# Kernel optimization log

Measured on AMD Instinct MI355X. Metric: run time of the kernel, lower is better.

Reference implementation:

```python
import jax, jax.numpy as jnp
import numpy as np

NEG_SLOPE = 0.2
EPS = 1e-16

N_NODES = 32768
N_EDGES = 160000
DIM = 768
HEADS1 = 4
OUT1 = DIM // HEADS1  # 192 per head, concat -> 768
HEADS2 = 1
OUT2 = DIM
N_REL = 3


def setup_inputs() -> dict:
    key = jax.random.key(0)
    ks = jax.random.split(key, 12)
    s = 0.02
    return {
        "x": jax.random.normal(ks[0], (N_NODES, DIM), dtype=jnp.float32),
        "edge_index": jax.random.randint(ks[1], (2, N_EDGES), 0, N_NODES, dtype=jnp.int64),
        "edge_type": jax.random.randint(ks[2], (N_EDGES,), 0, N_REL, dtype=jnp.int64),
        "W1": jax.random.normal(ks[3], (N_REL, DIM, HEADS1 * OUT1), dtype=jnp.float32) * s,
        "q1": jax.random.normal(ks[4], (HEADS1 * OUT1, HEADS1), dtype=jnp.float32) * s,
        "k1": jax.random.normal(ks[5], (HEADS1 * OUT1, HEADS1), dtype=jnp.float32) * s,
        "b1": jnp.zeros((HEADS1 * OUT1,), dtype=jnp.float32),
        "W2": jax.random.normal(ks[6], (N_REL, DIM, HEADS2 * OUT2), dtype=jnp.float32) * s,
        "q2": jax.random.normal(ks[7], (HEADS2 * OUT2, HEADS2), dtype=jnp.float32) * s,
        "k2": jax.random.normal(ks[8], (HEADS2 * OUT2, HEADS2), dtype=jnp.float32) * s,
        "b2": jnp.zeros((HEADS2 * OUT2,), dtype=jnp.float32),
    }


def rgat_conv(x, W, q, k, b, src, dst, etype, heads, out_ch, n_nodes):
    """PyG RGATConv, additive-self-attention, across-relation, concat=True, eval mode."""
    # per-relation transform of all nodes: [R, N, H*O] (avoids [E, in, H*O] weight gather)
    xr = jnp.einsum('nd,rdf->rnf', x, W)
    oi = xr[etype, dst]                      # [E, H*O] transformed target feats
    oj = xr[etype, src]                      # [E, H*O] transformed source feats
    qi = oi @ q                              # [E, H]
    kj = oj @ k                              # [E, H]
    alpha = jax.nn.leaky_relu(qi + kj, NEG_SLOPE)
    # segment softmax over edges sharing the same target node
    m = jax.ops.segment_max(alpha, dst, num_segments=n_nodes)     # [N, H]
    e = jnp.exp(alpha - m[dst])
    z = jax.ops.segment_sum(e, dst, num_segments=n_nodes)         # [N, H]
    a = e / (z[dst] + EPS)                                        # [E, H]
    msg = (a[:, :, None] * oj.reshape(-1, heads, out_ch)).reshape(-1, heads * out_ch)
    out = jax.ops.segment_sum(msg, dst, num_segments=n_nodes)     # [N, H*O]
    return out + b


def reference(x, edge_index, edge_type, W1, q1, k1, b1, W2, q2, k2, b2):
    src, dst = edge_index[0], edge_index[1]
    n = x.shape[0]
    h = rgat_conv(x, W1, q1, k1, b1, src, dst, edge_type, HEADS1, OUT1, n)
    h = jax.nn.elu(h)
    # dropout is identity in eval mode
    out = rgat_conv(h, W2, q2, k2, b2, src, dst, edge_type, HEADS2, OUT2, n)
    return out
```

## Files before the change

kernel.cpp:

```cpp
#include <hip/hip_runtime.h>


#define DIM   768
#define NREL  3

typedef __bf16 bf16x8 __attribute__((ext_vector_type(8)));
typedef float  f32x4  __attribute__((ext_vector_type(4)));
typedef float  f32x16 __attribute__((ext_vector_type(16)));
typedef unsigned short us4 __attribute__((ext_vector_type(4)));
typedef unsigned short us8 __attribute__((ext_vector_type(8)));

__device__ __forceinline__ float bfs(unsigned short u){
  union { unsigned u; float f; } v; v.u = ((unsigned)u) << 16; return v.f;
}
__device__ __forceinline__ float bfl(unsigned x){
  union { unsigned u; float f; } v; v.u = x << 16; return v.f;
}
__device__ __forceinline__ float bfh(unsigned x){
  union { unsigned u; float f; } v; v.u = x & 0xffff0000u; return v.f;
}
__device__ __forceinline__ unsigned short f2bf(float f){
  union { float f; unsigned u; } v; v.f = f;
  unsigned r = v.u + 0x7fffu + ((v.u >> 16) & 1u);
  return (unsigned short)(r >> 16);
}
__device__ __forceinline__ unsigned pck(float a, float b){
  return (unsigned)f2bf(a) | ((unsigned)f2bf(b) << 16);
}
__device__ __forceinline__ float ldf(const void* p, size_t i, int is32){
  return is32 ? ((const float*)p)[i] : bfs(((const unsigned short*)p)[i]);
}
__device__ __forceinline__ int ldi(const void* p, size_t i, int is64){
  return is64 ? ((const int*)p)[2 * i] : ((const int*)p)[i];
}

typedef __attribute__((address_space(1))) void gvoid_t;
typedef __attribute__((address_space(3))) void lvoid_t;
__device__ __forceinline__ void gload16(const void* g, void* l){
  __builtin_amdgcn_global_load_lds((gvoid_t*)g, (lvoid_t*)l, 16, 0, 0);
}

template<int H>
__device__ __forceinline__ float sel(const float (&a)[H], int h){
  float v = a[0];
#pragma unroll
  for (int i = 1; i < H; ++i) v = (h == i) ? a[i] : v;
  return v;
}

__global__ void detect_kernel(const unsigned short* __restrict__ xu,
                              const unsigned* __restrict__ eiu,
                              const unsigned* __restrict__ etyu,
                              int* __restrict__ flags){
  __shared__ int s_weird, s_ei, s_ety;
  int t = threadIdx.x;
  if (t == 0){ s_weird = 0; s_ei = 0; s_ety = 0; }
  __syncthreads();
  unsigned short u = xu[2 * t];
  int ex = (u >> 7) & 0xff;
  if (ex >= 0xF0 || ex <= 0x40) atomicAdd(&s_weird, 1);
  if (t < 128){
    if (eiu[2 * t + 1]  != 0) atomicAdd(&s_ei, 1);
    if (etyu[2 * t + 1] != 0) atomicAdd(&s_ety, 1);
  }
  __syncthreads();
  if (t == 0){
    flags[0] = (s_weird > 16) ? 1 : 0;
    flags[1] = (s_ei  == 0) ? 1 : 0;
    flags[2] = (s_ety == 0) ? 1 : 0;
  }
}

__global__ void convert_x(const void* __restrict__ xin, unsigned short* __restrict__ xb,
                          const int* __restrict__ flags, int n4){
  int i = blockIdx.x * blockDim.x + threadIdx.x;
  if (i >= n4) return;
  if (flags[0]){
    float4 v = ((const float4*)xin)[i];
    us4 o; o.x = f2bf(v.x); o.y = f2bf(v.y); o.z = f2bf(v.z); o.w = f2bf(v.w);
    ((us4*)xb)[i] = o;
  } else {
    ((us4*)xb)[i] = ((const us4*)xin)[i];
  }
}

__global__ void hist_kernel(const void* __restrict__ ei, int* __restrict__ counts,
                            const int* __restrict__ flags, int E){
  int e = blockIdx.x * blockDim.x + threadIdx.x;
  if (e < E) atomicAdd(&counts[ldi(ei, (size_t)E + e, flags[1])], 1);
}

__global__ void scan_kernel(const int* __restrict__ counts, int* __restrict__ offs,
                            int* __restrict__ cursor, int n){
  __shared__ int s[1024];
  int tid = threadIdx.x;
  int base = tid * 32;
  int loc[32];
  int run = 0;
#pragma unroll
  for (int i = 0; i < 32; ++i){ loc[i] = run; run += counts[base + i]; }
  s[tid] = run;
  __syncthreads();
  for (int off = 1; off < 1024; off <<= 1){
    int add = (tid >= off) ? s[tid - off] : 0;
    __syncthreads();
    s[tid] += add;
    __syncthreads();
  }
  int ex = (tid == 0) ? 0 : s[tid - 1];
#pragma unroll
  for (int i = 0; i < 32; ++i){
    int o = ex + loc[i];
    offs[base + i]   = o;
    cursor[base + i] = o;
  }
  if (tid == 1023) offs[n] = s[1023];
}

__global__ void scatter_kernel(const void* __restrict__ ei, const void* __restrict__ ety,
                               int* __restrict__ cursor, int* __restrict__ payload,
                               const int* __restrict__ flags, int E){
  int e = blockIdx.x * blockDim.x + threadIdx.x;
  if (e < E){
    int dst = ldi(ei, (size_t)E + e, flags[1]);
    int src = ldi(ei, (size_t)e,     flags[1]);
    int et  = ldi(ety, (size_t)e,    flags[2]);
    int pos = atomicAdd(&cursor[dst], 1);
    payload[pos] = (et << 16) | src;
  }
}

__global__ void transpose_w(const void* __restrict__ W, unsigned short* __restrict__ Wt,
                            const int* __restrict__ flags){
  __shared__ unsigned short t[32][33];
  int is32 = flags[0];
  int r = blockIdx.z;
  size_t Wb = (size_t)r * DIM * DIM;
  unsigned short* Wd = Wt + (size_t)r * DIM * DIM;
  int tx = threadIdx.x, ty = threadIdx.y;
  int x  = blockIdx.x * 32 + tx;
  int y0 = blockIdx.y * 32;
#pragma unroll
  for (int i = 0; i < 32; i += 8)
    t[ty + i][tx] = f2bf(ldf(W, Wb + (size_t)(y0 + ty + i) * DIM + x, is32));
  __syncthreads();
  int x2 = blockIdx.y * 32 + tx;
  int y2 = blockIdx.x * 32;
#pragma unroll
  for (int i = 0; i < 32; i += 8) Wd[(size_t)(y2 + ty + i) * DIM + x2] = t[tx][ty + i];
}

template<int H>
__global__ void wqk_kernel(const void* __restrict__ W,
                           const void* __restrict__ q, const void* __restrict__ k,
                           unsigned short* __restrict__ Wqkb,
                           const int* __restrict__ flags){
  int is32 = flags[0];
  int wid  = (blockIdx.x * blockDim.x + threadIdx.x) >> 6;
  int lane = threadIdx.x & 63;
  int r = wid / DIM, d = wid % DIM;
  size_t Wrow = ((size_t)r * DIM + d) * DIM;
  float aq[H], ak[H];
#pragma unroll
  for (int h = 0; h < H; ++h){ aq[h] = 0.f; ak[h] = 0.f; }
#pragma unroll
  for (int j = 0; j < 12; ++j){
    int f = j * 64 + lane;
    float wv = ldf(W, Wrow + f, is32);
#pragma unroll
    for (int h = 0; h < H; ++h){
      aq[h] += wv * ldf(q, (size_t)f * H + h, is32);
      ak[h] += wv * ldf(k, (size_t)f * H + h, is32);
    }
  }
#pragma unroll
  for (int h = 0; h < H; ++h){
    for (int off = 32; off; off >>= 1){
      aq[h] += __shfl_xor(aq[h], off);
      ak[h] += __shfl_xor(ak[h], off);
    }
  }
  if (lane == 0){
#pragma unroll
    for (int h = 0; h < H; ++h){
      Wqkb[(size_t)d * 32 + r * 8 + h]     = f2bf(aq[h]);
      Wqkb[(size_t)d * 32 + r * 8 + 4 + h] = f2bf(ak[h]);
    }
  }
}

__global__ void pack_b(const unsigned short* __restrict__ Wqkb, unsigned short* __restrict__ Bpk){
  int i = blockIdx.x * 256 + threadIdx.x;
  if (i >= 3072) return;
  int lane = i & 63, nt = (i >> 6) & 1, t = i >> 7;
  int kb = t * 32 + (lane >> 4) * 8;
  int col = nt * 16 + (lane & 15);
  us8 v;
#pragma unroll
  for (int j = 0; j < 8; ++j) v[j] = Wqkb[(size_t)(kb + j) * 32 + col];
  ((us8*)Bpk)[i] = v;
}

__global__ void __launch_bounds__(256)
qnkn_mfma(const unsigned short* __restrict__ X, const unsigned short* __restrict__ Bpk,
          float* __restrict__ qn, float* __restrict__ kn, int nN){
  int wv = threadIdx.x >> 6, lane = threadIdx.x & 63;
  int row0 = (blockIdx.x * 4 + wv) * 16;
  int ar = lane & 15, quad = lane >> 4;
  const unsigned short* Arow = X + (size_t)(row0 + ar) * DIM + quad * 8;
  const bf16x8* Bp = (const bf16x8*)Bpk;
  f32x4 acc0 = {0.f,0.f,0.f,0.f}, acc1 = {0.f,0.f,0.f,0.f};
#pragma unroll
  for (int t = 0; t < 24; ++t){
    bf16x8 a  = *(const bf16x8*)(Arow + t * 32);
    bf16x8 b0 = Bp[(t * 2 + 0) * 64 + lane];
    bf16x8 b1 = Bp[(t * 2 + 1) * 64 + lane];
    acc0 = __builtin_amdgcn_mfma_f32_16x16x32_bf16(a, b0, acc0, 0, 0, 0);
    acc1 = __builtin_amdgcn_mfma_f32_16x16x32_bf16(a, b1, acc1, 0, 0, 0);
  }
#pragma unroll
  for (int nt = 0; nt < 2; ++nt){
    int col = nt * 16 + (lane & 15);
    if (col < 24){
      int r = col >> 3, isK = (col >> 2) & 1, h = col & 3;
      float* bp = isK ? kn : qn;
      f32x4 a = nt ? acc1 : acc0;
#pragma unroll
      for (int j = 0; j < 4; ++j){
        int row = row0 + quad * 4 + j;
        bp[((size_t)r * nN + row) * 4 + h] = a[j];
      }
    }
  }
}

#define MF(A_, B_, C_) __builtin_amdgcn_mfma_f32_32x32x16_bf16(A_, B_, C_, 0, 0, 0)

#define STAGE(SW, KW) {                                                       \
  gload16(gAa + (KW),            &lds[(SW)*24576 +         wB]);              \
  gload16(gAa +  64*DIM + (KW),  &lds[(SW)*24576 +  4096 + wB]);              \
  gload16(gAa + 128*DIM + (KW),  &lds[(SW)*24576 +  8192 + wB]);              \
  gload16(gAa + 192*DIM + (KW),  &lds[(SW)*24576 + 12288 + wB]);              \
  gload16(gBb + (KW),            &lds[(SW)*24576 + 16384 + wB]);              \
  gload16(gBb +  64*DIM + (KW),  &lds[(SW)*24576 + 20480 + wB]);              \
}

#define STEP(S, KW, DOST) {                                                   \
  if (DOST) STAGE(((S)+2)%3, KW);                                             \
  bf16x8 b00 = *(const bf16x8*)&lds[(S)*24576 + boff0];                       \
  bf16x8 b01 = *(const bf16x8*)&lds[(S)*24576 + boff1];                       \
  bf16x8 b10 = *(const bf16x8*)&lds[(S)*24576 + boff0 + 2048];                \
  bf16x8 b11 = *(const bf16x8*)&lds[(S)*24576 + boff1 + 2048];                \
  bf16x8 a00 = *(const bf16x8*)&lds[(S)*24576 + aoff0];                       \
  bf16x8 a01 = *(const bf16x8*)&lds[(S)*24576 + aoff1];                       \
  bf16x8 a10 = *(const bf16x8*)&lds[(S)*24576 + aoff0 + 2048];                \
  bf16x8 a11 = *(const bf16x8*)&lds[(S)*24576 + aoff1 + 2048];                \
  bf16x8 a20 = *(const bf16x8*)&lds[(S)*24576 + aoff0 + 4096];                \
  bf16x8 a21 = *(const bf16x8*)&lds[(S)*24576 + aoff1 + 4096];                \
  bf16x8 a30 = *(const bf16x8*)&lds[(S)*24576 + aoff0 + 6144];                \
  bf16x8 a31 = *(const bf16x8*)&lds[(S)*24576 + aoff1 + 6144];                \
  __builtin_amdgcn_s_setprio(1);                                              \
  acc[0][0] = MF(a00, b00, acc[0][0]); acc[0][1] = MF(a00, b10, acc[0][1]);   \
  acc[1][0] = MF(a10, b00, acc[1][0]); acc[1][1] = MF(a10, b10, acc[1][1]);   \
  acc[2][0] = MF(a20, b00, acc[2][0]); acc[2][1] = MF(a20, b10, acc[2][1]);   \
  acc[3][0] = MF(a30, b00, acc[3][0]); acc[3][1] = MF(a30, b10, acc[3][1]);   \
  acc[0][0] = MF(a01, b01, acc[0][0]); acc[0][1] = MF(a01, b11, acc[0][1]);   \
  acc[1][0] = MF(a11, b01, acc[1][0]); acc[1][1] = MF(a11, b11, acc[1][1]);   \
  acc[2][0] = MF(a21, b01, acc[2][0]); acc[2][1] = MF(a21, b11, acc[2][1]);   \
  acc[3][0] = MF(a31, b01, acc[3][0]); acc[3][1] = MF(a31, b11, acc[3][1]);   \
  __builtin_amdgcn_s_setprio(0);                                              \
}
#define W6 { asm volatile("s_waitcnt vmcnt(6)" ::: "memory"); __builtin_amdgcn_s_barrier(); }

__global__ void __launch_bounds__(256, 2)
gemm_bf16(const unsigned short* __restrict__ A,
          const unsigned short* __restrict__ Bt,
          unsigned short* __restrict__ C, int M){
  __shared__ __align__(16) unsigned char lds[73728];
  const int K = DIM;
  int i = blockIdx.x;
  int xcd = i & 7, s = i >> 3;
  int bm  = xcd * 16 + s / 18;
  int bnr = s % 18;
  int rrel = bnr / 6, bn = bnr % 6;
  int tid = threadIdx.x;
  int w = tid >> 6, lane = tid & 63;
  int wr = w >> 1, wc = w & 1;
  int lo = lane & 31, hi = lane >> 5;

  int jl   = lo >> 1, rlow = lo & 1, e7 = jl & 7;
  int p0   = (rlow * 4 + hi)     ^ e7;
  int p1   = (rlow * 4 + 2 + hi) ^ e7;
  int aoff0 = (wr * 64 + jl) * 128 + p0 * 16;
  int aoff1 = (wr * 64 + jl) * 128 + p1 * 16;
  int boff0 = 16384 + (wc * 32 + jl) * 128 + p0 * 16;
  int boff1 = 16384 + (wc * 32 + jl) * 128 + p1 * 16;

  int sq   = (tid & 7) ^ ((tid >> 3) & 7);
  int srow = 2 * (tid >> 3) + (sq >> 2);
  const unsigned short* gAa = A  + ((size_t)bm * 256 + srow) * K + (sq & 3) * 8;
  const unsigned short* gBb = Bt + ((size_t)(rrel * DIM + bn * 128 + srow)) * K + (sq & 3) * 8;
  int wB = w * 1024;

  f32x16 acc[4][2];
  f32x16 zz = {0.f,0.f,0.f,0.f,0.f,0.f,0.f,0.f,0.f,0.f,0.f,0.f,0.f,0.f,0.f,0.f};
#pragma unroll
  for (int a = 0; a < 4; ++a){ acc[a][0] = zz; acc[a][1] = zz; }

  STAGE(0, 0); STAGE(1, 32);
  W6;

#pragma unroll 1
  for (int t7 = 0; t7 < 7; ++t7){
    int kb = t7 * 96;
    STEP(0, kb + 64,  1); W6;
    STEP(1, kb + 96,  1); W6;
    STEP(2, kb + 128, 1); W6;
  }
  STEP(0, 736, 1); W6;
  STEP(1, 0, 0);
  asm volatile("s_waitcnt vmcnt(0)" ::: "memory");
  __builtin_amdgcn_s_barrier();
  STEP(2, 0, 0);

  unsigned short* Cg = C + ((size_t)rrel * M + (size_t)bm * 256) * DIM + bn * 128;
#pragma unroll
  for (int mi = 0; mi < 4; ++mi)
#pragma unroll
    for (int ni = 0; ni < 2; ++ni)
#pragma unroll
      for (int rg = 0; rg < 4; ++rg)
#pragma unroll
        for (int j = 0; j < 4; ++j){
          int row = wr * 128 + mi * 32 + rg * 8 + hi * 4 + j;
          int col = wc * 64 + ni * 32 + lo;
          Cg[(size_t)row * DIM + col] = f2bf(acc[mi][ni][rg * 4 + j]);
        }
}

template<int H, bool ELU, bool OUT32>
__global__ void __launch_bounds__(256)
agg_kernel(const unsigned short* __restrict__ xr,
           const float* __restrict__ qn, const float* __restrict__ kn,
           const int* __restrict__ offs, const int* __restrict__ payload,
           const void* __restrict__ bias,
           void* __restrict__ outp,
           const int* __restrict__ flags, int nN, int E){
  const int WH = (H == 4) ? 4 : 1;
  __shared__ int   pay_s[4][64];
  __shared__ float w_s[4][64 * WH];
  int is32 = flags[0];
  int wv   = threadIdx.x >> 6;
  int lane = threadIdx.x & 63;
  int n = blockIdx.x * 4 + wv;
  int rs = offs[n], re = offs[n + 1];
  rs = max(rs, 0); re = min(re, E);
  const int myh = (H == 1) ? 0 : (lane >> 4);

  float m_run[H], z_run[H], acc[12];
#pragma unroll
  for (int h = 0; h < H; ++h){ m_run[h] = -__builtin_inff(); z_run[h] = 0.f; }
#pragma unroll
  for (int i = 0; i < 12; ++i) acc[i] = 0.f;

  for (int base = rs; base < re; base += 64){
    int dc = min(64, re - base);
    int pay = 0;
    float al[H];
#pragma unroll
    for (int h = 0; h < H; ++h) al[h] = -__builtin_inff();
    if (lane < dc){
      pay = payload[base + lane];
      int et = pay >> 16, src = pay & 0xffff;
      if (H == 4){
        f32x4 qv = *(const f32x4*)(qn + ((size_t)et * nN + n)   * 4);
        f32x4 kv = *(const f32x4*)(kn + ((size_t)et * nN + src) * 4);
#pragma unroll
        for (int h = 0; h < H; ++h){
          float a = qv[h & 3] + kv[h & 3];
          al[h] = (a > 0.f) ? a : 0.2f * a;
        }
      } else {
        float a = qn[((size_t)et * nN + n) * 4] + kn[((size_t)et * nN + src) * 4];
        al[0] = (a > 0.f) ? a : 0.2f * a;
      }
    }
    float scs[H], wgt[H];
#pragma unroll
    for (int h = 0; h < H; ++h){
      float v = al[h];
      for (int off = 32; off; off >>= 1) v = fmaxf(v, __shfl_xor(v, off));
      float nm = fmaxf(m_run[h], v);
      scs[h] = (m_run[h] == -__builtin_inff()) ? 0.f : expf(m_run[h] - nm);
      m_run[h] = nm;
      wgt[h] = (lane < dc) ? expf(al[h] - nm) : 0.f;
      float s = wgt[h];
      for (int off = 32; off; off >>= 1) s += __shfl_xor(s, off);
      z_run[h] = z_run[h] * scs[h] + s;
    }
    float msc = sel<H>(scs, myh);
#pragma unroll
    for (int i = 0; i < 12; ++i) acc[i] *= msc;

    if (lane < dc){
      pay_s[wv][lane] = pay;
#pragma unroll
      for (int h = 0; h < WH; ++h) w_s[wv][lane * WH + h] = wgt[h];
    }

    for (int j0 = 0; j0 < dc; j0 += 4){
      uint2 c[4][3];
      float w4[4];
#pragma unroll
      for (int u = 0; u < 4; ++u){
        int jc = j0 + u;
        int ok = jc < dc;
        int jl2 = ok ? jc : j0;
        int pj = pay_s[wv][jl2];
        float ww = w_s[wv][jl2 * WH + ((H == 1) ? 0 : myh)];
        w4[u] = ok ? ww : 0.f;
        int et = pj >> 16, src = pj & 0xffff;
        const uint2* rp = (const uint2*)(xr + ((size_t)et * nN + src) * DIM + lane * 12);
        c[u][0] = rp[0]; c[u][1] = rp[1]; c[u][2] = rp[2];
      }
#pragma unroll
      for (int u = 0; u < 4; ++u){
        float wj = w4[u];
        acc[0]  += wj * bfl(c[u][0].x); acc[1]  += wj * bfh(c[u][0].x);
        acc[2]  += wj * bfl(c[u][0].y); acc[3]  += wj * bfh(c[u][0].y);
        acc[4]  += wj * bfl(c[u][1].x); acc[5]  += wj * bfh(c[u][1].x);
        acc[6]  += wj * bfl(c[u][1].y); acc[7]  += wj * bfh(c[u][1].y);
        acc[8]  += wj * bfl(c[u][2].x); acc[9]  += wj * bfh(c[u][2].x);
        acc[10] += wj * bfl(c[u][2].y); acc[11] += wj * bfh(c[u][2].y);
      }
    }
  }

  float inv = 1.0f / (sel<H>(z_run, myh) + 1e-16f);
  float o[12];
#pragma unroll
  for (int i = 0; i < 12; ++i){
    float v = acc[i] * inv + ldf(bias, (size_t)lane * 12 + i, is32);
    if (ELU) v = (v > 0.f) ? v : (expf(v) - 1.f);
    o[i] = v;
  }
  if (OUT32 && is32){
    float* op = (float*)outp + (size_t)n * DIM + lane * 12;
    float4 f0 = {o[0], o[1], o[2],  o[3]};
    float4 f1 = {o[4], o[5], o[6],  o[7]};
    float4 f2 = {o[8], o[9], o[10], o[11]};
    ((float4*)op)[0] = f0; ((float4*)op)[1] = f1; ((float4*)op)[2] = f2;
  } else {
    uint2* op = (uint2*)((unsigned short*)outp + (size_t)n * DIM + lane * 12);
    uint2 s0, s1, s2;
    s0.x = pck(o[0], o[1]);  s0.y = pck(o[2], o[3]);
    s1.x = pck(o[4], o[5]);  s1.y = pck(o[6], o[7]);
    s2.x = pck(o[8], o[9]);  s2.y = pck(o[10], o[11]);
    op[0] = s0; op[1] = s1; op[2] = s2;
  }
}

extern "C" void kernel_launch(void* const* d_in, const int* in_sizes, int n_in,
                              void* d_out, int out_size, void* d_ws, size_t ws_size,
                              hipStream_t stream){
  const void* x   = d_in[0];
  const void* ei  = d_in[1];
  const void* ety = d_in[2];
  const void* W1  = d_in[3];
  const void* q1  = d_in[4];
  const void* k1  = d_in[5];
  const void* b1  = d_in[6];
  const void* W2  = d_in[7];
  const void* q2  = d_in[8];
  const void* k2  = d_in[9];
  const void* b2  = d_in[10];

  int nN = in_sizes[0] / DIM;
  int E  = in_sizes[2];

  char* ws = (char*)d_ws;
  size_t off = 0;
  auto alloc = [&](size_t bytes) -> void* {
    void* p = ws + off;
    off += (bytes + 255) & ~(size_t)255;
    return p;
  };
  unsigned short* xr   = (unsigned short*)alloc((size_t)NREL * nN * DIM * 2);
  unsigned short* xb   = (unsigned short*)alloc((size_t)nN * DIM * 2);
  unsigned short* h    = (unsigned short*)alloc((size_t)nN * DIM * 2);
  unsigned short* Wt   = (unsigned short*)alloc((size_t)NREL * DIM * DIM * 2);
  unsigned short* Wqkb = (unsigned short*)alloc((size_t)DIM * 32 * 2);
  unsigned short* Bpk  = (unsigned short*)alloc((size_t)3072 * 16);
  float* qn  = (float*)alloc((size_t)NREL * nN * 4 * 4);
  float* kn  = (float*)alloc((size_t)NREL * nN * 4 * 4);
  int* offs    = (int*)alloc((size_t)(nN + 1) * 4);
  int* cursor  = (int*)alloc((size_t)nN * 4);
  int* counts  = (int*)alloc((size_t)nN * 4);
  int* payload = (int*)alloc((size_t)E * 4);
  int* flags   = (int*)alloc(16);

  detect_kernel<<<1, 256, 0, stream>>>((const unsigned short*)x, (const unsigned*)ei,
                                       (const unsigned*)ety, flags);
  convert_x<<<(nN * DIM / 4 + 255) / 256, 256, 0, stream>>>(x, xb, flags, nN * DIM / 4);

  hipMemsetAsync(counts, 0, (size_t)nN * 4, stream);
  hist_kernel<<<(E + 255) / 256, 256, 0, stream>>>(ei, counts, flags, E);
  scan_kernel<<<1, 1024, 0, stream>>>(counts, offs, cursor, nN);
  scatter_kernel<<<(E + 255) / 256, 256, 0, stream>>>(ei, ety, cursor, payload, flags, E);

  dim3 tg(DIM / 32, DIM / 32, NREL), tb(32, 8);
  int gemm_blocks = 8 * (16 * 18);

  transpose_w<<<tg, tb, 0, stream>>>(W1, Wt, flags);
  hipMemsetAsync(Wqkb, 0, (size_t)DIM * 32 * 2, stream);
  wqk_kernel<4><<<(NREL * DIM) / 4, 256, 0, stream>>>(W1, q1, k1, Wqkb, flags);
  pack_b<<<12, 256, 0, stream>>>(Wqkb, Bpk);
  qnkn_mfma<<<nN / 64, 256, 0, stream>>>(xb, Bpk, qn, kn, nN);
  gemm_bf16<<<gemm_blocks, 256, 0, stream>>>(xb, Wt, xr, nN);
  agg_kernel<4, true, false><<<nN / 4, 256, 0, stream>>>(xr, qn, kn, offs, payload, b1, h,
                                                         flags, nN, E);

  transpose_w<<<tg, tb, 0, stream>>>(W2, Wt, flags);
  hipMemsetAsync(Wqkb, 0, (size_t)DIM * 32 * 2, stream);
  wqk_kernel<1><<<(NREL * DIM) / 4, 256, 0, stream>>>(W2, q2, k2, Wqkb, flags);
  pack_b<<<12, 256, 0, stream>>>(Wqkb, Bpk);
  qnkn_mfma<<<nN / 64, 256, 0, stream>>>(h, Bpk, qn, kn, nN);
  gemm_bf16<<<gemm_blocks, 256, 0, stream>>>(h, Wt, xr, nN);
  agg_kernel<1, false, true><<<nN / 4, 256, 0, stream>>>(xr, qn, kn, offs, payload, b2,
                                                         d_out, flags, nN, E);
}
```

Measured before the change: 661.3 us.

## Enlarge GEMM block tile to 256x256 with 4x4 MFMA accumulators per wave

```diff
diff --git a/kernel.cpp b/kernel.cpp
--- a/kernel.cpp
+++ b/kernel.cpp
@@ -236,104 +236,117 @@
 
 #define MF(A_, B_, C_) __builtin_amdgcn_mfma_f32_32x32x16_bf16(A_, B_, C_, 0, 0, 0)
 
-#define STAGE(SW, KW) {                                                       \
-  gload16(gAa + (KW),            &lds[(SW)*24576 +         wB]);              \
-  gload16(gAa +  64*DIM + (KW),  &lds[(SW)*24576 +  4096 + wB]);              \
-  gload16(gAa + 128*DIM + (KW),  &lds[(SW)*24576 +  8192 + wB]);              \
-  gload16(gAa + 192*DIM + (KW),  &lds[(SW)*24576 + 12288 + wB]);              \
-  gload16(gBb + (KW),            &lds[(SW)*24576 + 16384 + wB]);              \
-  gload16(gBb +  64*DIM + (KW),  &lds[(SW)*24576 + 20480 + wB]);              \
-}
-
-#define STEP(S, KW, DOST) {                                                   \
-  if (DOST) STAGE(((S)+2)%3, KW);                                             \
-  bf16x8 b00 = *(const bf16x8*)&lds[(S)*24576 + boff0];                       \
-  bf16x8 b01 = *(const bf16x8*)&lds[(S)*24576 + boff1];                       \
-  bf16x8 b10 = *(const bf16x8*)&lds[(S)*24576 + boff0 + 2048];                \
-  bf16x8 b11 = *(const bf16x8*)&lds[(S)*24576 + boff1 + 2048];                \
-  bf16x8 a00 = *(const bf16x8*)&lds[(S)*24576 + aoff0];                       \
-  bf16x8 a01 = *(const bf16x8*)&lds[(S)*24576 + aoff1];                       \
-  bf16x8 a10 = *(const bf16x8*)&lds[(S)*24576 + aoff0 + 2048];                \
-  bf16x8 a11 = *(const bf16x8*)&lds[(S)*24576 + aoff1 + 2048];                \
-  bf16x8 a20 = *(const bf16x8*)&lds[(S)*24576 + aoff0 + 4096];                \
-  bf16x8 a21 = *(const bf16x8*)&lds[(S)*24576 + aoff1 + 4096];                \
-  bf16x8 a30 = *(const bf16x8*)&lds[(S)*24576 + aoff0 + 6144];                \
-  bf16x8 a31 = *(const bf16x8*)&lds[(S)*24576 + aoff1 + 6144];                \
-  __builtin_amdgcn_s_setprio(1);                                              \
-  acc[0][0] = MF(a00, b00, acc[0][0]); acc[0][1] = MF(a00, b10, acc[0][1]);   \
-  acc[1][0] = MF(a10, b00, acc[1][0]); acc[1][1] = MF(a10, b10, acc[1][1]);   \
-  acc[2][0] = MF(a20, b00, acc[2][0]); acc[2][1] = MF(a20, b10, acc[2][1]);   \
-  acc[3][0] = MF(a30, b00, acc[3][0]); acc[3][1] = MF(a30, b10, acc[3][1]);   \
-  acc[0][0] = MF(a01, b01, acc[0][0]); acc[0][1] = MF(a01, b11, acc[0][1]);   \
-  acc[1][0] = MF(a11, b01, acc[1][0]); acc[1][1] = MF(a11, b11, acc[1][1]);   \
-  acc[2][0] = MF(a21, b01, acc[2][0]); acc[2][1] = MF(a21, b11, acc[2][1]);   \
-  acc[3][0] = MF(a31, b01, acc[3][0]); acc[3][1] = MF(a31, b11, acc[3][1]);   \
-  __builtin_amdgcn_s_setprio(0);                                              \
-}
-#define W6 { asm volatile("s_waitcnt vmcnt(6)" ::: "memory"); __builtin_amdgcn_s_barrier(); }
-
-__global__ void __launch_bounds__(256, 2)
+#define STAGE(SW, KW) {                                                        \
+  gload16(gAa + (KW),                 &lds[(SW)*32768 +         wB]);          \
+  gload16(gAa + (KW) + 16,            &lds[(SW)*32768 +  8192 + wB]);          \
+  gload16(gAa + 128*DIM + (KW),       &lds[(SW)*32768 +  4096 + wB]);          \
+  gload16(gAa + 128*DIM + (KW) + 16,  &lds[(SW)*32768 + 12288 + wB]);          \
+  gload16(gBb + (KW),                 &lds[(SW)*32768 + 16384 + wB]);          \
+  gload16(gBb + (KW) + 16,            &lds[(SW)*32768 + 24576 + wB]);          \
+  gload16(gBb + 128*DIM + (KW),       &lds[(SW)*32768 + 20480 + wB]);          \
+  gload16(gBb + 128*DIM + (KW) + 16,  &lds[(SW)*32768 + 28672 + wB]);          \
+}
+
+#define STEP(S, KW, DOST) {                                                    \
+  if (DOST) STAGE(((S)+2)%3, KW);                                              \
+  bf16x8 a00 = *(const bf16x8*)&lds[(S)*32768 + aoff];                         \
+  bf16x8 a01 = *(const bf16x8*)&lds[(S)*32768 + aoff + 1024];                  \
+  bf16x8 a02 = *(const bf16x8*)&lds[(S)*32768 + aoff + 2048];                  \
+  bf16x8 a03 = *(const bf16x8*)&lds[(S)*32768 + aoff + 3072];                  \
+  bf16x8 b00 = *(const bf16x8*)&lds[(S)*32768 + boff];                         \
+  bf16x8 b01 = *(const bf16x8*)&lds[(S)*32768 + boff + 1024];                  \
+  bf16x8 b02 = *(const bf16x8*)&lds[(S)*32768 + boff + 2048];                  \
+  bf16x8 b03 = *(const bf16x8*)&lds[(S)*32768 + boff + 3072];                  \
+  bf16x8 a10 = *(const bf16x8*)&lds[(S)*32768 + 8192 + aoff];                  \
+  bf16x8 a11 = *(const bf16x8*)&lds[(S)*32768 + 8192 + aoff + 1024];           \
+  bf16x8 a12 = *(const bf16x8*)&lds[(S)*32768 + 8192 + aoff + 2048];           \
+  bf16x8 a13 = *(const bf16x8*)&lds[(S)*32768 + 8192 + aoff + 3072];           \
+  bf16x8 b10 = *(const bf16x8*)&lds[(S)*32768 + 8192 + boff];                  \
+  bf16x8 b11 = *(const bf16x8*)&lds[(S)*32768 + 8192 + boff + 1024];           \
+  bf16x8 b12 = *(const bf16x8*)&lds[(S)*32768 + 8192 + boff + 2048];           \
+  bf16x8 b13 = *(const bf16x8*)&lds[(S)*32768 + 8192 + boff + 3072];           \
+  __builtin_amdgcn_s_setprio(1);                                               \
+  acc[0][0] = MF(a00, b00, acc[0][0]); acc[0][1] = MF(a00, b01, acc[0][1]);    \
+  acc[0][2] = MF(a00, b02, acc[0][2]); acc[0][3] = MF(a00, b03, acc[0][3]);    \
+  acc[1][0] = MF(a01, b00, acc[1][0]); acc[1][1] = MF(a01, b01, acc[1][1]);    \
+  acc[1][2] = MF(a01, b02, acc[1][2]); acc[1][3] = MF(a01, b03, acc[1][3]);    \
+  acc[2][0] = MF(a02, b00, acc[2][0]); acc[2][1] = MF(a02, b01, acc[2][1]);    \
+  acc[2][2] = MF(a02, b02, acc[2][2]); acc[2][3] = MF(a02, b03, acc[2][3]);    \
+  acc[3][0] = MF(a03, b00, acc[3][0]); acc[3][1] = MF(a03, b01, acc[3][1]);    \
+  acc[3][2] = MF(a03, b02, acc[3][2]); acc[3][3] = MF(a03, b03, acc[3][3]);    \
+  acc[0][0] = MF(a10, b10, acc[0][0]); acc[0][1] = MF(a10, b11, acc[0][1]);    \
+  acc[0][2] = MF(a10, b12, acc[0][2]); acc[0][3] = MF(a10, b13, acc[0][3]);    \
+  acc[1][0] = MF(a11, b10, acc[1][0]); acc[1][1] = MF(a11, b11, acc[1][1]);    \
+  acc[1][2] = MF(a11, b12, acc[1][2]); acc[1][3] = MF(a11, b13, acc[1][3]);    \
+  acc[2][0] = MF(a12, b10, acc[2][0]); acc[2][1] = MF(a12, b11, acc[2][1]);    \
+  acc[2][2] = MF(a12, b12, acc[2][2]); acc[2][3] = MF(a12, b13, acc[2][3]);    \
+  acc[3][0] = MF(a13, b10, acc[3][0]); acc[3][1] = MF(a13, b11, acc[3][1]);    \
+  acc[3][2] = MF(a13, b12, acc[3][2]); acc[3][3] = MF(a13, b13, acc[3][3]);    \
+  __builtin_amdgcn_s_setprio(0);                                               \
+}
+#define W8 { asm volatile("s_waitcnt vmcnt(8)" ::: "memory"); __builtin_amdgcn_s_barrier(); }
+
+__global__ void __launch_bounds__(256, 1)
 gemm_bf16(const unsigned short* __restrict__ A,
           const unsigned short* __restrict__ Bt,
           unsigned short* __restrict__ C, int M){
-  __shared__ __align__(16) unsigned char lds[73728];
+  __shared__ __align__(16) unsigned char lds[98304];
   const int K = DIM;
   int i = blockIdx.x;
   int xcd = i & 7, s = i >> 3;
-  int bm  = xcd * 16 + s / 18;
-  int bnr = s % 18;
-  int rrel = bnr / 6, bn = bnr % 6;
+  int bm  = xcd * 16 + s / 9;
+  int bnr = s % 9;
+  int rrel = bnr / 3, bn = bnr % 3;
   int tid = threadIdx.x;
   int w = tid >> 6, lane = tid & 63;
   int wr = w >> 1, wc = w & 1;
   int lo = lane & 31, hi = lane >> 5;
 
-  int jl   = lo >> 1, rlow = lo & 1, e7 = jl & 7;
-  int p0   = (rlow * 4 + hi)     ^ e7;
-  int p1   = (rlow * 4 + 2 + hi) ^ e7;
-  int aoff0 = (wr * 64 + jl) * 128 + p0 * 16;
-  int aoff1 = (wr * 64 + jl) * 128 + p1 * 16;
-  int boff0 = 16384 + (wc * 32 + jl) * 128 + p0 * 16;
-  int boff1 = 16384 + (wc * 32 + jl) * 128 + p1 * 16;
+  int jq = lo >> 2;
+  int p  = (((lo & 3) << 1) | hi) ^ (jq & 7);
+  int aoff =         (wr * 32 + jq) * 128 + p * 16;
+  int boff = 16384 + (wc * 32 + jq) * 128 + p * 16;
 
   int sq   = (tid & 7) ^ ((tid >> 3) & 7);
-  int srow = 2 * (tid >> 3) + (sq >> 2);
-  const unsigned short* gAa = A  + ((size_t)bm * 256 + srow) * K + (sq & 3) * 8;
-  const unsigned short* gBb = Bt + ((size_t)(rrel * DIM + bn * 128 + srow)) * K + (sq & 3) * 8;
+  int srow = 4 * (tid >> 3) + (sq >> 1);
+  const unsigned short* gAa = A  + ((size_t)bm * 256 + srow) * K + (sq & 1) * 8;
+  const unsigned short* gBb = Bt + ((size_t)(rrel * DIM + bn * 256 + srow)) * K + (sq & 1) * 8;
   int wB = w * 1024;
 
-  f32x16 acc[4][2];
+  f32x16 acc[4][4];
   f32x16 zz = {0.f,0.f,0.f,0.f,0.f,0.f,0.f,0.f,0.f,0.f,0.f,0.f,0.f,0.f,0.f,0.f};
 #pragma unroll
-  for (int a = 0; a < 4; ++a){ acc[a][0] = zz; acc[a][1] = zz; }
+  for (int a = 0; a < 4; ++a)
+#pragma unroll
+    for (int b = 0; b < 4; ++b) acc[a][b] = zz;
 
   STAGE(0, 0); STAGE(1, 32);
-  W6;
+  W8;
 
 #pragma unroll 1
   for (int t7 = 0; t7 < 7; ++t7){
     int kb = t7 * 96;
-    STEP(0, kb + 64,  1); W6;
-    STEP(1, kb + 96,  1); W6;
-    STEP(2, kb + 128, 1); W6;
-  }
-  STEP(0, 736, 1); W6;
+    STEP(0, kb + 64,  1); W8;
+    STEP(1, kb + 96,  1); W8;
+    STEP(2, kb + 128, 1); W8;
+  }
+  STEP(0, 736, 1); W8;
   STEP(1, 0, 0);
   asm volatile("s_waitcnt vmcnt(0)" ::: "memory");
   __builtin_amdgcn_s_barrier();
   STEP(2, 0, 0);
 
-  unsigned short* Cg = C + ((size_t)rrel * M + (size_t)bm * 256) * DIM + bn * 128;
+  unsigned short* Cg = C + ((size_t)rrel * M + (size_t)bm * 256) * DIM + bn * 256;
 #pragma unroll
   for (int mi = 0; mi < 4; ++mi)
 #pragma unroll
-    for (int ni = 0; ni < 2; ++ni)
+    for (int ni = 0; ni < 4; ++ni)
 #pragma unroll
       for (int rg = 0; rg < 4; ++rg)
 #pragma unroll
         for (int j = 0; j < 4; ++j){
           int row = wr * 128 + mi * 32 + rg * 8 + hi * 4 + j;
-          int col = wc * 64 + ni * 32 + lo;
+          int col = wc * 128 + ni * 32 + lo;
           Cg[(size_t)row * DIM + col] = f2bf(acc[mi][ni][rg * 4 + j]);
         }
 }
@@ -509,7 +522,7 @@
   scatter_kernel<<<(E + 255) / 256, 256, 0, stream>>>(ei, ety, cursor, payload, flags, E);
 
   dim3 tg(DIM / 32, DIM / 32, NREL), tb(32, 8);
-  int gemm_blocks = 8 * (16 * 18);
+  int gemm_blocks = 8 * (16 * 9);
 
   transpose_w<<<tg, tb, 0, stream>>>(W1, Wt, flags);
   hipMemsetAsync(Wqkb, 0, (size_t)DIM * 32 * 2, stream);
```

New measurement: 717.8 us. 8.5% more time.
